# Performance work log

Hardware: AMD Instinct MI355X
Metric: run time of the kernel (lower is better)

The kernel has to match this reference:

```python
import jax, jax.numpy as jnp
import numpy as np

N_NODES = 50000
N_EDGES = 800000
IN_DIM = 128
HID = 128
OUT_DIM = 40
N_LAYERS = 4
N_GRAPHS = 128
BN_EPS = 1e-5


def setup_inputs() -> dict:
    key = jax.random.key(0)
    ks = jax.random.split(key, 12)
    sc1 = 1.0 / np.sqrt(HID)
    inp = {
        "x": jax.random.normal(ks[0], (N_NODES, IN_DIM), jnp.float32),
        "edge_index": jax.random.randint(ks[1], (2, N_EDGES), 0, N_NODES, jnp.int64),
        "batch": jnp.sort(jax.random.randint(ks[2], (N_NODES,), 0, N_GRAPHS, jnp.int64)),
        "W1s": jax.random.normal(ks[3], (N_LAYERS, IN_DIM, HID), jnp.float32) * sc1,
        "b1s": jnp.zeros((N_LAYERS, HID), jnp.float32),
        "W2s": jax.random.normal(ks[4], (N_LAYERS, HID, HID), jnp.float32) * sc1,
        "b2s": jnp.zeros((N_LAYERS, HID), jnp.float32),
        "gammas": jnp.ones((N_LAYERS, HID), jnp.float32),
        "betas": jnp.zeros((N_LAYERS, HID), jnp.float32),
        "bn_means": jax.random.normal(ks[5], (N_LAYERS, HID), jnp.float32) * 0.1,
        "bn_vars": jax.random.uniform(ks[6], (N_LAYERS, HID), jnp.float32, 0.5, 1.5),
        "eps_arr": jnp.zeros((N_LAYERS,), jnp.float32),
        "lin1_W": jax.random.normal(ks[7], (HID, HID), jnp.float32) * sc1,
        "lin1_b": jnp.zeros((HID,), jnp.float32),
        "lin2_W": jax.random.normal(ks[8], (HID, OUT_DIM), jnp.float32) * sc1,
        "lin2_b": jnp.zeros((OUT_DIM,), jnp.float32),
    }
    return inp


def _gin_forward(x, edge_index, batch, W1s, b1s, W2s, b2s, gammas, betas,
                 bn_means, bn_vars, eps_arr, lin1_W, lin1_b, lin2_W, lin2_b):
    src, dst = edge_index[0], edge_index[1]
    n = x.shape[0]
    for i in range(N_LAYERS):
        # GINConv: MLP((1+eps)*x_i + sum_{j->i} x_j)
        agg = jax.ops.segment_sum(x[src], dst, num_segments=n)  # [N, d]
        h = (1.0 + eps_arr[i]) * x + agg
        h = jax.nn.relu(h @ W1s[i] + b1s[i])
        h = jax.nn.relu(h @ W2s[i] + b2s[i])
        # BatchNorm1d (inference: running stats)
        x = gammas[i] * (h - bn_means[i]) * jax.lax.rsqrt(bn_vars[i] + BN_EPS) + betas[i]
    # global mean pool per graph
    sums = jax.ops.segment_sum(x, batch, num_segments=N_GRAPHS)  # [G, HID]
    counts = jax.ops.segment_sum(jnp.ones((n,), x.dtype), batch, num_segments=N_GRAPHS)
    pooled = sums / jnp.maximum(counts, 1.0)[:, None]
    h = jax.nn.relu(pooled @ lin1_W + lin1_b)
    # dropout is identity in eval mode
    logits = h @ lin2_W + lin2_b
    return jax.nn.log_softmax(logits, axis=-1)


def reference(x, edge_index, batch, W1s, b1s, W2s, b2s, gammas, betas,
              bn_means, bn_vars, eps_arr, lin1_W, lin1_b, lin2_W, lin2_b):
    return _gin_forward(x, edge_index, batch, W1s, b1s, W2s, b2s, gammas, betas,
                        bn_means, bn_vars, eps_arr, lin1_W, lin1_b, lin2_W, lin2_b)
```

## Files before the change

### kernel.cpp

```cpp
#include <hip/hip_runtime.h>
#include <hip/hip_bf16.h>
#include <math.h>

#define N_NODES  50000
#define N_EDGES  800000
#define HID      128
#define OUT_DIM  40
#define N_LAYERS 4
#define N_GRAPHS 128
#define BN_EPS   1e-5f
#define TROWS    32
#define LSTRIDE  136
#define CAP      64

typedef short v8s __attribute__((ext_vector_type(8)));
typedef float v4f __attribute__((ext_vector_type(4)));
typedef unsigned v4u __attribute__((ext_vector_type(4)));

static __device__ __forceinline__ short f2bf(float f) {
    __hip_bfloat16 h = __float2bfloat16(f);
    return __builtin_bit_cast(short, h);
}
static __device__ __forceinline__ float bflo(unsigned u) {
    return __builtin_bit_cast(float, u << 16);
}
static __device__ __forceinline__ float bfhi(unsigned u) {
    return __builtin_bit_cast(float, u & 0xffff0000u);
}
static __device__ __forceinline__ unsigned packbf(float a0, float a1) {
    return ((unsigned)(unsigned short)f2bf(a1) << 16) | (unsigned)(unsigned short)f2bf(a0);
}

__global__ __launch_bounds__(256) void k_pre(const float* __restrict__ x,
                                             unsigned* __restrict__ xb,
                                             const int* __restrict__ src,
                                             const int* __restrict__ dst,
                                             int* __restrict__ cursor,
                                             unsigned short* __restrict__ csr,
                                             const float* __restrict__ W1s,
                                             const float* __restrict__ W2s,
                                             const float* __restrict__ lin1,
                                             const float* __restrict__ lin2,
                                             short* __restrict__ Wp) {
    int b = blockIdx.x, t = threadIdx.x;
    if (b < 782) {
        int base = b * 1024;
#pragma unroll
        for (int k = 0; k < 4; k++) {
            int e = base + t + k * 256;
            if (e < N_EDGES) {
                int d = dst[e];
                int p = atomicAdd(&cursor[d], 1);
                if (p < CAP) csr[d * CAP + p] = (unsigned short)src[e];
            }
        }
    } else if (b < 3907) {
        int j = (b - 782) * 256 + t;
        const float4* x4 = (const float4*)x;
        float4 f0 = x4[2 * j];
        float4 f1 = x4[2 * j + 1];
        uint4 o;
        o.x = packbf(f0.x, f0.y);
        o.y = packbf(f0.z, f0.w);
        o.z = packbf(f1.x, f1.y);
        o.w = packbf(f1.z, f1.w);
        ((uint4*)xb)[j] = o;
    } else {
        int bp = b - 3907;
        if (bp < 9) {
            const float* W = (bp < 4) ? (W1s + bp * 16384)
                           : (bp < 8) ? (W2s + (bp - 4) * 16384)
                                      : lin1;
            short* o = Wp + (size_t)bp * 16384;
#pragma unroll
            for (int i = 0; i < 8; i++) {
                int c = i * 256 + t;
                int f = c >> 6, lane = c & 63;
                int ks = f >> 3, nt = f & 7;
                int k0 = ks * 32 + (lane >> 4) * 8;
                int n  = nt * 16 + (lane & 15);
                union { v8s v; short s[8]; } u;
#pragma unroll
                for (int j = 0; j < 8; j++) u.s[j] = f2bf(W[(k0 + j) * 128 + n]);
                *(v8s*)(o + (size_t)c * 8) = u.v;
            }
        } else {
            short* o = Wp + (size_t)9 * 16384;
#pragma unroll
            for (int i = 0; i < 3; i++) {
                int c = i * 256 + t;
                if (c < 768) {
                    int f = c >> 6, lane = c & 63;
                    int ks = f / 3, nt = f % 3;
                    int k0 = ks * 32 + (lane >> 4) * 8;
                    int n  = nt * 16 + (lane & 15);
                    union { v8s v; short s[8]; } u;
#pragma unroll
                    for (int j = 0; j < 8; j++)
                        u.s[j] = (n < OUT_DIM) ? f2bf(lin2[(k0 + j) * OUT_DIM + n]) : (short)0;
                    *(v8s*)(o + (size_t)(ks * 8 + nt) * 8 * 64 + (size_t)lane * 8) = u.v;
                }
            }
        }
    }
}

__global__ __launch_bounds__(256) void k_mlp(const short* __restrict__ xb,
                                             const unsigned short* __restrict__ csr,
                                             const int* __restrict__ deg,
                                             const short* __restrict__ Wp1,
                                             const short* __restrict__ Wp2,
                                             const float* __restrict__ b1,
                                             const float* __restrict__ b2,
                                             const float* __restrict__ gamma,
                                             const float* __restrict__ beta,
                                             const float* __restrict__ mean,
                                             const float* __restrict__ var,
                                             const float* __restrict__ eps_arr,
                                             int layer,
                                             short* __restrict__ out,
                                             int N) {
    __shared__ __align__(16) short H[TROWS * LSTRIDE];
    int tid = threadIdx.x, lane = tid & 63, w = tid >> 6;
    int m16 = lane & 15, quad = lane >> 4;
    int rbase = blockIdx.x * TROWS;

    {
        float sc = 1.0f + eps_arr[layer];
        const v4u* X4 = (const v4u*)xb;
        int g = lane >> 4, sub = lane & 15;
        for (int i = w; i < TROWS; i += 4) {
            int r = rbase + i;
            if (r >= N) {
                if (g == 0) {
                    v4u z = {0u, 0u, 0u, 0u};
                    *(v4u*)&H[i * LSTRIDE + sub * 8] = z;
                }
                continue;
            }
            int cnt = min(deg[r], CAP);
            int idx = (lane < cnt) ? (int)csr[r * CAP + lane] : 0;
            float a0 = 0.f, a1 = 0.f, a2 = 0.f, a3 = 0.f;
            float a4 = 0.f, a5 = 0.f, a6 = 0.f, a7 = 0.f;
            for (int j = 0; j < cnt; j += 8) {
                int e0 = j + g, e1 = j + 4 + g;
                float m0 = (e0 < cnt) ? 1.0f : 0.0f;
                float m1 = (e1 < cnt) ? 1.0f : 0.0f;
                int s0 = __shfl(idx, e0, 64);
                int s1 = __shfl(idx, e1, 64);
                v4u u0 = X4[(size_t)s0 * 16 + sub];
                v4u u1 = X4[(size_t)s1 * 16 + sub];
                a0 += m0 * bflo(u0.x); a1 += m0 * bfhi(u0.x);
                a2 += m0 * bflo(u0.y); a3 += m0 * bfhi(u0.y);
                a4 += m0 * bflo(u0.z); a5 += m0 * bfhi(u0.z);
                a6 += m0 * bflo(u0.w); a7 += m0 * bfhi(u0.w);
                a0 += m1 * bflo(u1.x); a1 += m1 * bfhi(u1.x);
                a2 += m1 * bflo(u1.y); a3 += m1 * bfhi(u1.y);
                a4 += m1 * bflo(u1.z); a5 += m1 * bfhi(u1.z);
                a6 += m1 * bflo(u1.w); a7 += m1 * bfhi(u1.w);
            }
            a0 += __shfl_xor(a0, 16, 64); a0 += __shfl_xor(a0, 32, 64);
            a1 += __shfl_xor(a1, 16, 64); a1 += __shfl_xor(a1, 32, 64);
            a2 += __shfl_xor(a2, 16, 64); a2 += __shfl_xor(a2, 32, 64);
            a3 += __shfl_xor(a3, 16, 64); a3 += __shfl_xor(a3, 32, 64);
            a4 += __shfl_xor(a4, 16, 64); a4 += __shfl_xor(a4, 32, 64);
            a5 += __shfl_xor(a5, 16, 64); a5 += __shfl_xor(a5, 32, 64);
            a6 += __shfl_xor(a6, 16, 64); a6 += __shfl_xor(a6, 32, 64);
            a7 += __shfl_xor(a7, 16, 64); a7 += __shfl_xor(a7, 32, 64);
            if (g == 0) {
                v4u us = X4[(size_t)r * 16 + sub];
                a0 += sc * bflo(us.x); a1 += sc * bfhi(us.x);
                a2 += sc * bflo(us.y); a3 += sc * bfhi(us.y);
                a4 += sc * bflo(us.z); a5 += sc * bfhi(us.z);
                a6 += sc * bflo(us.w); a7 += sc * bfhi(us.w);
                v4u o;
                o.x = packbf(a0, a1); o.y = packbf(a2, a3);
                o.z = packbf(a4, a5); o.w = packbf(a6, a7);
                *(v4u*)&H[i * LSTRIDE + sub * 8] = o;
            }
        }
    }
    __syncthreads();

    float pb1[2], pb2[2], ps[2], pt[2];
#pragma unroll
    for (int nt = 0; nt < 2; nt++) {
        int c = w * 32 + nt * 16 + m16;
        pb1[nt] = b1[c];
        pb2[nt] = b2[c];
        float g = gamma[c];
        float iv = rsqrtf(var[c] + BN_EPS);
        ps[nt] = g * iv;
        pt[nt] = beta[c] - g * mean[c] * iv;
    }

    v4f acc[2][2];
#pragma unroll
    for (int mt = 0; mt < 2; mt++)
#pragma unroll
        for (int nt = 0; nt < 2; nt++) acc[mt][nt] = {0.f, 0.f, 0.f, 0.f};

#pragma unroll
    for (int ks = 0; ks < 4; ks++) {
        v8s bfr[2];
#pragma unroll
        for (int nt = 0; nt < 2; nt++)
            bfr[nt] = ((const v8s*)Wp1)[(ks * 8 + w * 2 + nt) * 64 + lane];
#pragma unroll
        for (int mt = 0; mt < 2; mt++) {
            v8s a = *(const v8s*)&H[(mt * 16 + m16) * LSTRIDE + ks * 32 + quad * 8];
#pragma unroll
            for (int nt = 0; nt < 2; nt++)
                acc[mt][nt] = __builtin_amdgcn_mfma_f32_16x16x32_bf16(a, bfr[nt], acc[mt][nt], 0, 0, 0);
        }
    }
    __syncthreads();

#pragma unroll
    for (int mt = 0; mt < 2; mt++)
#pragma unroll
        for (int nt = 0; nt < 2; nt++)
#pragma unroll
            for (int r4 = 0; r4 < 4; r4++) {
                float y = fmaxf(acc[mt][nt][r4] + pb1[nt], 0.f);
                H[(mt * 16 + quad * 4 + r4) * LSTRIDE + w * 32 + nt * 16 + m16] = f2bf(y);
            }
    __syncthreads();

    v4f acc2[2][2];
#pragma unroll
    for (int mt = 0; mt < 2; mt++)
#pragma unroll
        for (int nt = 0; nt < 2; nt++) acc2[mt][nt] = {0.f, 0.f, 0.f, 0.f};

#pragma unroll
    for (int ks = 0; ks < 4; ks++) {
        v8s bfr[2];
#pragma unroll
        for (int nt = 0; nt < 2; nt++)
            bfr[nt] = ((const v8s*)Wp2)[(ks * 8 + w * 2 + nt) * 64 + lane];
#pragma unroll
        for (int mt = 0; mt < 2; mt++) {
            v8s a = *(const v8s*)&H[(mt * 16 + m16) * LSTRIDE + ks * 32 + quad * 8];
#pragma unroll
            for (int nt = 0; nt < 2; nt++)
                acc2[mt][nt] = __builtin_amdgcn_mfma_f32_16x16x32_bf16(a, bfr[nt], acc2[mt][nt], 0, 0, 0);
        }
    }

#pragma unroll
    for (int mt = 0; mt < 2; mt++)
#pragma unroll
        for (int r4 = 0; r4 < 4; r4++) {
            int row = rbase + mt * 16 + quad * 4 + r4;
            if (row < N) {
#pragma unroll
                for (int nt = 0; nt < 2; nt++) {
                    float y = fmaxf(acc2[mt][nt][r4] + pb2[nt], 0.f);
                    y = ps[nt] * y + pt[nt];
                    out[(size_t)row * HID + w * 32 + nt * 16 + m16] = f2bf(y);
                }
            }
        }
}

__global__ __launch_bounds__(256) void k_pool(const short* __restrict__ Xs,
                                              const int* __restrict__ batch,
                                              short* __restrict__ pooled) {
    int g = blockIdx.x;
    int tid = threadIdx.x, lane = tid & 63, w = tid >> 6;
    __shared__ int sh[2];
    __shared__ float red0[256], red1[256];
    if (tid < 2) {
        int target = g + tid;
        int lo = 0, hi = N_NODES;
        while (lo < hi) {
            int mid = (lo + hi) >> 1;
            if (batch[mid] < target) lo = mid + 1; else hi = mid;
        }
        sh[tid] = lo;
    }
    __syncthreads();
    int lo = sh[0], hi = sh[1];
    const unsigned* X = (const unsigned*)Xs;
    float a0 = 0.f, a1 = 0.f;
    for (int r = lo + w; r < hi; r += 4) {
        unsigned u = X[(size_t)r * 64 + lane];
        a0 += bflo(u);
        a1 += bfhi(u);
    }
    red0[tid] = a0;
    red1[tid] = a1;
    __syncthreads();
    if (w == 0) {
        float s0 = red0[lane] + red0[64 + lane] + red0[128 + lane] + red0[192 + lane];
        float s1 = red1[lane] + red1[64 + lane] + red1[128 + lane] + red1[192 + lane];
        float c = fmaxf((float)(hi - lo), 1.0f);
        ((unsigned*)pooled)[g * 64 + lane] = packbf(s0 / c, s1 / c);
    }
}

__global__ __launch_bounds__(256) void k_head(const short* __restrict__ pooled,
                                              const short* __restrict__ Wp8,
                                              const short* __restrict__ Wp9,
                                              const float* __restrict__ b1h,
                                              const float* __restrict__ b2h,
                                              float* __restrict__ out) {
    __shared__ __align__(16) short Hl[128 * LSTRIDE];
    __shared__ float Ll[128 * OUT_DIM];
    int tid = threadIdx.x, lane = tid & 63, w = tid >> 6;
    int m16 = lane & 15, quad = lane >> 4;

    {
        int nh = w & 1, mh = w >> 1, base = mh * 64;
        float pb[4];
#pragma unroll
        for (int nt = 0; nt < 4; nt++) pb[nt] = b1h[nh * 64 + nt * 16 + m16];
        v4f acc[4][4];
#pragma unroll
        for (int mt = 0; mt < 4; mt++)
#pragma unroll
            for (int nt = 0; nt < 4; nt++) acc[mt][nt] = {0.f, 0.f, 0.f, 0.f};
#pragma unroll
        for (int ks = 0; ks < 4; ks++) {
            v8s bfr[4];
#pragma unroll
            for (int nt = 0; nt < 4; nt++)
                bfr[nt] = ((const v8s*)Wp8)[(ks * 8 + nh * 4 + nt) * 64 + lane];
#pragma unroll
            for (int mt = 0; mt < 4; mt++) {
                v8s a = *(const v8s*)(pooled + (size_t)(base + mt * 16 + m16) * HID
                                      + ks * 32 + quad * 8);
#pragma unroll
                for (int nt = 0; nt < 4; nt++)
                    acc[mt][nt] = __builtin_amdgcn_mfma_f32_16x16x32_bf16(a, bfr[nt], acc[mt][nt], 0, 0, 0);
            }
        }
#pragma unroll
        for (int mt = 0; mt < 4; mt++)
#pragma unroll
            for (int r4 = 0; r4 < 4; r4++) {
                int row = base + mt * 16 + quad * 4 + r4;
#pragma unroll
                for (int nt = 0; nt < 4; nt++)
                    Hl[row * LSTRIDE + nh * 64 + nt * 16 + m16] =
                        f2bf(fmaxf(acc[mt][nt][r4] + pb[nt], 0.f));
            }
    }
    __syncthreads();

    {
        v4f acc[2][3];
#pragma unroll
        for (int mt = 0; mt < 2; mt++)
#pragma unroll
            for (int nt = 0; nt < 3; nt++) acc[mt][nt] = {0.f, 0.f, 0.f, 0.f};
#pragma unroll
        for (int ks = 0; ks < 4; ks++) {
            v8s bfr[3];
#pragma unroll
            for (int nt = 0; nt < 3; nt++)
                bfr[nt] = ((const v8s*)Wp9)[(ks * 8 + nt) * 64 + lane];
#pragma unroll
            for (int mt = 0; mt < 2; mt++) {
                v8s a = *(const v8s*)&Hl[(w * 32 + mt * 16 + m16) * LSTRIDE + ks * 32 + quad * 8];
#pragma unroll
                for (int nt = 0; nt < 3; nt++)
                    acc[mt][nt] = __builtin_amdgcn_mfma_f32_16x16x32_bf16(a, bfr[nt], acc[mt][nt], 0, 0, 0);
            }
        }
#pragma unroll
        for (int mt = 0; mt < 2; mt++)
#pragma unroll
            for (int r4 = 0; r4 < 4; r4++) {
                int row = w * 32 + mt * 16 + quad * 4 + r4;
#pragma unroll
                for (int nt = 0; nt < 3; nt++) {
                    int col = nt * 16 + m16;
                    if (col < OUT_DIM)
                        Ll[row * OUT_DIM + col] = acc[mt][nt][r4] + b2h[col];
                }
            }
    }
    __syncthreads();

    for (int g = w; g < N_GRAPHS; g += 4) {
        float a = (lane < OUT_DIM) ? Ll[g * OUT_DIM + lane] : -INFINITY;
        float v = a;
        for (int d = 32; d > 0; d >>= 1) v = fmaxf(v, __shfl_xor(v, d, 64));
        float ex = (lane < OUT_DIM) ? expf(a - v) : 0.0f;
        float s = ex;
        for (int d = 32; d > 0; d >>= 1) s += __shfl_xor(s, d, 64);
        if (lane < OUT_DIM) out[g * OUT_DIM + lane] = a - v - logf(s);
    }
}

extern "C" void kernel_launch(void* const* d_in, const int* in_sizes, int n_in,
                              void* d_out, int out_size, void* d_ws, size_t ws_size,
                              hipStream_t stream) {
    const float* x       = (const float*)d_in[0];
    const int*   edge    = (const int*)d_in[1];
    const int*   batch   = (const int*)d_in[2];
    const float* W1s     = (const float*)d_in[3];
    const float* b1s     = (const float*)d_in[4];
    const float* W2s     = (const float*)d_in[5];
    const float* b2s     = (const float*)d_in[6];
    const float* gammas  = (const float*)d_in[7];
    const float* betas   = (const float*)d_in[8];
    const float* bn_m    = (const float*)d_in[9];
    const float* bn_v    = (const float*)d_in[10];
    const float* eps_arr = (const float*)d_in[11];
    const float* lin1_W  = (const float*)d_in[12];
    const float* lin1_b  = (const float*)d_in[13];
    const float* lin2_W  = (const float*)d_in[14];
    const float* lin2_b  = (const float*)d_in[15];

    const int* src = edge;
    const int* dst = edge + N_EDGES;

    short* bufA    = (short*)d_ws;
    short* bufB    = bufA + (size_t)N_NODES * HID;
    short* Wp      = bufB + (size_t)N_NODES * HID;
    short* pooled  = Wp + 10 * 16384;
    int*   cursor  = (int*)(pooled + N_GRAPHS * HID);
    unsigned short* csr = (unsigned short*)(cursor + N_NODES);

    (void)hipMemsetAsync(cursor, 0, N_NODES * sizeof(int), stream);
    k_pre<<<3917, 256, 0, stream>>>(x, (unsigned*)bufA, src, dst, cursor, csr,
                                    W1s, W2s, lin1_W, lin2_W, Wp);

    const int mlpBlocks = (N_NODES + TROWS - 1) / TROWS;
    short* in   = bufA;
    short* outb = bufB;
    for (int l = 0; l < N_LAYERS; l++) {
        k_mlp<<<mlpBlocks, 256, 0, stream>>>(in, csr, cursor,
                                             Wp + (size_t)l * 16384,
                                             Wp + (size_t)(4 + l) * 16384,
                                             b1s + l * HID, b2s + l * HID,
                                             gammas + l * HID, betas + l * HID,
                                             bn_m + l * HID, bn_v + l * HID,
                                             eps_arr, l, outb, N_NODES);
        short* tmp = in; in = outb; outb = tmp;
    }

    k_pool<<<N_GRAPHS, 256, 0, stream>>>(in, batch, pooled);
    k_head<<<1, 256, 0, stream>>>(pooled, Wp + (size_t)8 * 16384, Wp + (size_t)9 * 16384,
                                  lin1_b, lin2_b, (float*)d_out);
}
```

Measured before the change: 335.2 us.

## Split pooling across blocks with atomics and widen neighbor gather unroll

```diff
diff --git a/kernel.cpp b/kernel.cpp
--- a/kernel.cpp
+++ b/kernel.cpp
@@ -12,6 +12,7 @@
 #define TROWS    32
 #define LSTRIDE  136
 #define CAP      64
+#define POOL_P   8
 
 typedef short v8s __attribute__((ext_vector_type(8)));
 typedef float v4f __attribute__((ext_vector_type(4)));
@@ -142,14 +143,20 @@
             int idx = (lane < cnt) ? (int)csr[r * CAP + lane] : 0;
             float a0 = 0.f, a1 = 0.f, a2 = 0.f, a3 = 0.f;
             float a4 = 0.f, a5 = 0.f, a6 = 0.f, a7 = 0.f;
-            for (int j = 0; j < cnt; j += 8) {
-                int e0 = j + g, e1 = j + 4 + g;
+            for (int j = 0; j < cnt; j += 16) {
+                int e0 = j + g, e1 = j + 4 + g, e2 = j + 8 + g, e3 = j + 12 + g;
                 float m0 = (e0 < cnt) ? 1.0f : 0.0f;
                 float m1 = (e1 < cnt) ? 1.0f : 0.0f;
+                float m2 = (e2 < cnt) ? 1.0f : 0.0f;
+                float m3 = (e3 < cnt) ? 1.0f : 0.0f;
                 int s0 = __shfl(idx, e0, 64);
                 int s1 = __shfl(idx, e1, 64);
+                int s2 = __shfl(idx, e2, 64);
+                int s3 = __shfl(idx, e3, 64);
                 v4u u0 = X4[(size_t)s0 * 16 + sub];
                 v4u u1 = X4[(size_t)s1 * 16 + sub];
+                v4u u2 = X4[(size_t)s2 * 16 + sub];
+                v4u u3 = X4[(size_t)s3 * 16 + sub];
                 a0 += m0 * bflo(u0.x); a1 += m0 * bfhi(u0.x);
                 a2 += m0 * bflo(u0.y); a3 += m0 * bfhi(u0.y);
                 a4 += m0 * bflo(u0.z); a5 += m0 * bfhi(u0.z);
@@ -158,6 +165,14 @@
                 a2 += m1 * bflo(u1.y); a3 += m1 * bfhi(u1.y);
                 a4 += m1 * bflo(u1.z); a5 += m1 * bfhi(u1.z);
                 a6 += m1 * bflo(u1.w); a7 += m1 * bfhi(u1.w);
+                a0 += m2 * bflo(u2.x); a1 += m2 * bfhi(u2.x);
+                a2 += m2 * bflo(u2.y); a3 += m2 * bfhi(u2.y);
+                a4 += m2 * bflo(u2.z); a5 += m2 * bfhi(u2.z);
+                a6 += m2 * bflo(u2.w); a7 += m2 * bfhi(u2.w);
+                a0 += m3 * bflo(u3.x); a1 += m3 * bfhi(u3.x);
+                a2 += m3 * bflo(u3.y); a3 += m3 * bfhi(u3.y);
+                a4 += m3 * bflo(u3.z); a5 += m3 * bfhi(u3.z);
+                a6 += m3 * bflo(u3.w); a7 += m3 * bfhi(u3.w);
             }
             a0 += __shfl_xor(a0, 16, 64); a0 += __shfl_xor(a0, 32, 64);
             a1 += __shfl_xor(a1, 16, 64); a1 += __shfl_xor(a1, 32, 64);
@@ -266,8 +281,8 @@
 
 __global__ __launch_bounds__(256) void k_pool(const short* __restrict__ Xs,
                                               const int* __restrict__ batch,
-                                              short* __restrict__ pooled) {
-    int g = blockIdx.x;
+                                              float* __restrict__ pooledF) {
+    int g = blockIdx.x >> 3, part = blockIdx.x & 7;
     int tid = threadIdx.x, lane = tid & 63, w = tid >> 6;
     __shared__ int sh[2];
     __shared__ float red0[256], red1[256];
@@ -284,7 +299,7 @@
     int lo = sh[0], hi = sh[1];
     const unsigned* X = (const unsigned*)Xs;
     float a0 = 0.f, a1 = 0.f;
-    for (int r = lo + w; r < hi; r += 4) {
+    for (int r = lo + part * 4 + w; r < hi; r += 32) {
         unsigned u = X[(size_t)r * 64 + lane];
         a0 += bflo(u);
         a1 += bfhi(u);
@@ -295,21 +310,41 @@
     if (w == 0) {
         float s0 = red0[lane] + red0[64 + lane] + red0[128 + lane] + red0[192 + lane];
         float s1 = red1[lane] + red1[64 + lane] + red1[128 + lane] + red1[192 + lane];
-        float c = fmaxf((float)(hi - lo), 1.0f);
-        ((unsigned*)pooled)[g * 64 + lane] = packbf(s0 / c, s1 / c);
-    }
-}
-
-__global__ __launch_bounds__(256) void k_head(const short* __restrict__ pooled,
+        if (s0 != 0.f || s1 != 0.f) {
+            atomicAdd(&pooledF[g * HID + lane * 2], s0);
+            atomicAdd(&pooledF[g * HID + lane * 2 + 1], s1);
+        }
+    }
+}
+
+__global__ __launch_bounds__(256) void k_head(const float* __restrict__ pooledF,
+                                              const int* __restrict__ batch,
                                               const short* __restrict__ Wp8,
                                               const short* __restrict__ Wp9,
                                               const float* __restrict__ b1h,
                                               const float* __restrict__ b2h,
                                               float* __restrict__ out) {
+    __shared__ __align__(16) short Al[128 * LSTRIDE];
     __shared__ __align__(16) short Hl[128 * LSTRIDE];
     __shared__ float Ll[128 * OUT_DIM];
+    __shared__ float invc[N_GRAPHS];
     int tid = threadIdx.x, lane = tid & 63, w = tid >> 6;
     int m16 = lane & 15, quad = lane >> 4;
+
+    if (tid < N_GRAPHS) {
+        int g = tid, lo = 0, hi = N_NODES;
+        while (lo < hi) { int m = (lo + hi) >> 1; if (batch[m] < g) lo = m + 1; else hi = m; }
+        int s = lo; lo = 0; hi = N_NODES;
+        while (lo < hi) { int m = (lo + hi) >> 1; if (batch[m] < g + 1) lo = m + 1; else hi = m; }
+        invc[g] = 1.0f / fmaxf((float)(lo - s), 1.0f);
+    }
+    __syncthreads();
+
+    for (int i = tid; i < N_GRAPHS * HID; i += 256) {
+        int row = i >> 7, col = i & 127;
+        Al[row * LSTRIDE + col] = f2bf(pooledF[i] * invc[row]);
+    }
+    __syncthreads();
 
     {
         int nh = w & 1, mh = w >> 1, base = mh * 64;
@@ -329,8 +364,7 @@
                 bfr[nt] = ((const v8s*)Wp8)[(ks * 8 + nh * 4 + nt) * 64 + lane];
 #pragma unroll
             for (int mt = 0; mt < 4; mt++) {
-                v8s a = *(const v8s*)(pooled + (size_t)(base + mt * 16 + m16) * HID
-                                      + ks * 32 + quad * 8);
+                v8s a = *(const v8s*)&Al[(base + mt * 16 + m16) * LSTRIDE + ks * 32 + quad * 8];
 #pragma unroll
                 for (int nt = 0; nt < 4; nt++)
                     acc[mt][nt] = __builtin_amdgcn_mfma_f32_16x16x32_bf16(a, bfr[nt], acc[mt][nt], 0, 0, 0);
@@ -421,11 +455,11 @@
     short* bufA    = (short*)d_ws;
     short* bufB    = bufA + (size_t)N_NODES * HID;
     short* Wp      = bufB + (size_t)N_NODES * HID;
-    short* pooled  = Wp + 10 * 16384;
-    int*   cursor  = (int*)(pooled + N_GRAPHS * HID);
-    unsigned short* csr = (unsigned short*)(cursor + N_NODES);
-
-    (void)hipMemsetAsync(cursor, 0, N_NODES * sizeof(int), stream);
+    int*   cursor  = (int*)(Wp + 10 * 16384);
+    float* pooledF = (float*)(cursor + N_NODES);
+    unsigned short* csr = (unsigned short*)(pooledF + N_GRAPHS * HID);
+
+    (void)hipMemsetAsync(cursor, 0, (N_NODES + N_GRAPHS * HID) * sizeof(int), stream);
     k_pre<<<3917, 256, 0, stream>>>(x, (unsigned*)bufA, src, dst, cursor, csr,
                                     W1s, W2s, lin1_W, lin2_W, Wp);
 
@@ -443,7 +477,8 @@
         short* tmp = in; in = outb; outb = tmp;
     }
 
-    k_pool<<<N_GRAPHS, 256, 0, stream>>>(in, batch, pooled);
-    k_head<<<1, 256, 0, stream>>>(pooled, Wp + (size_t)8 * 16384, Wp + (size_t)9 * 16384,
-                                  lin1_b, lin2_b, (float*)d_out);
-}
+    k_pool<<<N_GRAPHS * POOL_P, 256, 0, stream>>>(in, batch, pooledF);
+    k_head<<<1, 256, 0, stream>>>(pooledF, batch, Wp + (size_t)8 * 16384,
+                                  Wp + (size_t)9 * 16384, lin1_b, lin2_b,
+                                  (float*)d_out);
+}
```

Result: slower. 352.5 us (+5.1%).
